# Kernel tuning notes

Measured on AMD Instinct MI355X. Metric: run time of the kernel, lower is better.

Reference implementation:

```python
import jax, jax.numpy as jnp
import numpy as np

B, T, HID, H, DH, K = 2, 1024, 1024, 16, 64, 4
ROPE_BASE = 10000.0
EPS = 1e-6


def _causal_dwconv(x, w, b):
    # x: (B, T, C); w: (C, 1, K) depthwise; causal left-pad K-1, then SiLU
    xc = jnp.transpose(x, (0, 2, 1))  # (B, C, T)
    y = jax.lax.conv_general_dilated(
        xc, w, window_strides=(1,), padding=[(K - 1, 0)],
        dimension_numbers=('NCH', 'OIH', 'NCH'), feature_group_count=xc.shape[1])
    y = y + b[None, :, None]
    return jax.nn.silu(jnp.transpose(y, (0, 2, 1)))


def _rope(x, cos, sin):
    # x: (B, T, H, D); cos/sin: (T, D) with emb = cat(freqs, freqs)
    c = cos[None, :, None, :]
    s = sin[None, :, None, :]
    x1, x2 = x[..., ::2], x[..., 1::2]
    return jnp.concatenate(
        [x1 * c[..., ::2] - x2 * s[..., ::2],
         x1 * s[..., ::2] + x2 * c[..., ::2]], axis=-1)


def _delta_rule(q, k, v, alpha, beta, D_param):
    # q,k,v: (B,T,H,DH); alpha,beta: (B,T,H)
    # S_t = alpha_t * (I - beta_t k_t k_t^T) S_{t-1} + beta_t k_t v_t^T
    # o_t  = q_t^T S_t-1-style readout + D * (q.k) * v   (matches torch einsum 'bhd,bhde->bhe')
    qs = jnp.moveaxis(q, 1, 0).astype(jnp.float32)  # (T,B,H,DH)
    ks = jnp.moveaxis(k, 1, 0).astype(jnp.float32)
    vs = jnp.moveaxis(v, 1, 0).astype(jnp.float32)
    als = jnp.moveaxis(alpha, 1, 0).astype(jnp.float32)  # (T,B,H)
    bes = jnp.moveaxis(beta, 1, 0).astype(jnp.float32)

    def step(S, inp):
        qt, kt, vt, at, bt = inp
        ot = jnp.einsum('bhd,bhde->bhe', qt, S)
        ot = ot + D_param[None, :, None] * jnp.sum(qt * kt, -1, keepdims=True) * vt
        kS = jnp.einsum('bhd,bhde->bhe', kt, S)  # k^T S
        at_ = at[..., None, None]
        bt_ = bt[..., None, None]
        S_new = at_ * (S - bt_ * kt[..., :, None] * kS[..., None, :]) \
                + bt_ * kt[..., :, None] * vt[..., None, :]
        return S_new, ot

    S0 = jnp.zeros((q.shape[0], H, DH, DH), jnp.float32)
    _, outs = jax.lax.scan(step, S0, (qs, ks, vs, als, bes))
    return jnp.moveaxis(outs, 0, 1)  # (B,T,H,DH)


def _forward(x, Wq, Wk, Wv, Wg, Wo, bw, bb, gkw, gkb,
             qcw, qcb, kcw, kcb, vcw, vcb, A_log, D_param, dt_bias, onorm_w):
    Bb, Tt, _ = x.shape
    q = _causal_dwconv(x @ Wq, qcw, qcb).reshape(Bb, Tt, H, DH)
    k = _causal_dwconv(x @ Wk, kcw, kcb).reshape(Bb, Tt, H, DH)
    v = _causal_dwconv(x @ Wv, vcw, vcb).reshape(Bb, Tt, H, DH)

    # RoPE (computed on the fly, fp32)
    t = jnp.arange(Tt, dtype=jnp.float32)
    inv_freq = 1.0 / (ROPE_BASE ** (jnp.arange(0, DH, 2, dtype=jnp.float32) / DH))
    freqs = jnp.outer(t, inv_freq)
    emb = jnp.concatenate([freqs, freqs], -1)
    cos, sin = jnp.cos(emb), jnp.sin(emb)
    q = _rope(q, cos, sin)
    k = _rope(k, cos, sin)

    # L2-normalize q/k (delta-net stability, NOT softmax)
    q = q * jax.lax.rsqrt(jnp.sum(q * q, -1, keepdims=True) + EPS)
    k = k * jax.lax.rsqrt(jnp.sum(k * k, -1, keepdims=True) + EPS)

    beta = jax.nn.sigmoid(x @ bw + bb)  # (B,T,H) writing strength
    alpha = jnp.exp(-jnp.exp(A_log) * jax.nn.softplus(x @ gkw + gkb + dt_bias))  # (B,T,H) decay

    o = _delta_rule(q, k, v, alpha, beta, D_param)  # (B,T,H,DH)

    # gated RMSNorm output: g * silu(RMSNorm(o))
    g = (x @ Wg).reshape(Bb, Tt, H, DH)
    on = o * jax.lax.rsqrt(jnp.mean(o * o, -1, keepdims=True) + EPS) * onorm_w
    o = g * jax.nn.silu(on)
    return o.reshape(Bb, Tt, H * DH) @ Wo


def setup_inputs() -> dict:
    key = jax.random.key(0)
    ks = jax.random.split(key, 20)
    w = lambda i, shape, s=0.02: (jax.random.normal(ks[i], shape, jnp.float32) * s)
    return {
        'x': jax.random.normal(ks[0], (B, T, HID), jnp.float32),
        'Wq': w(1, (HID, H * DH)), 'Wk': w(2, (HID, H * DH)),
        'Wv': w(3, (HID, H * DH)), 'Wg': w(4, (HID, H * DH)),
        'Wo': w(5, (H * DH, HID)),
        'bw': w(6, (HID, H)), 'bb': jnp.zeros((H,), jnp.float32),
        'gkw': w(7, (HID, H)), 'gkb': jnp.zeros((H,), jnp.float32),
        'qcw': w(8, (H * DH, 1, K), 0.3), 'qcb': jnp.zeros((H * DH,), jnp.float32),
        'kcw': w(9, (H * DH, 1, K), 0.3), 'kcb': jnp.zeros((H * DH,), jnp.float32),
        'vcw': w(10, (H * DH, 1, K), 0.3), 'vcb': jnp.zeros((H * DH,), jnp.float32),
        'A_log': jnp.log(jax.random.uniform(ks[11], (H,), jnp.float32, 1.0, 16.0)),
        'D_param': jnp.ones((H,), jnp.float32),
        'dt_bias': jax.random.uniform(ks[12], (H,), jnp.float32, -0.01, 0.01),
        'onorm_w': jnp.ones((DH,), jnp.float32),
    }


def reference(x, Wq, Wk, Wv, Wg, Wo, bw, bb, gkw, gkb,
              qcw, qcb, kcw, kcb, vcw, vcb, A_log, D_param, dt_bias, onorm_w):
    return _forward(x, Wq, Wk, Wv, Wg, Wo, bw, bb, gkw, gkb,
                    qcw, qcb, kcw, kcb, vcw, vcb, A_log, D_param, dt_bias, onorm_w)
```

## Files before the change

kernel.cpp:

```cpp
#include <hip/hip_runtime.h>
#include <hip/hip_bf16.h>
#include <cstdint>

#define T_LEN 1024
#define HIDN  1024
#define NH    16
#define DHD   64

typedef __bf16 bf16x8 __attribute__((ext_vector_type(8)));
typedef float  f32x4  __attribute__((ext_vector_type(4)));

__device__ inline void split8(float4 x0, float4 x1, uint4& hi, uint4& lo) {
  union { __bf16 h[8]; uint4 u; } ph, pl;
  float v[8] = {x0.x, x0.y, x0.z, x0.w, x1.x, x1.y, x1.z, x1.w};
#pragma unroll
  for (int j = 0; j < 8; j++) {
    __bf16 h = (__bf16)v[j];
    ph.h[j] = h;
    pl.h[j] = (__bf16)(v[j] - (float)h);
  }
  hi = ph.u; lo = pl.u;
}

__global__ __launch_bounds__(256) void k_transp_split(
    const float* __restrict__ W0, const float* __restrict__ W1,
    const float* __restrict__ W2, const float* __restrict__ W3,
    const float* __restrict__ W4,
    __bf16* __restrict__ H0, __bf16* __restrict__ H1, __bf16* __restrict__ H2,
    __bf16* __restrict__ H3, __bf16* __restrict__ H4,
    __bf16* __restrict__ L0, __bf16* __restrict__ L1, __bf16* __restrict__ L2,
    __bf16* __restrict__ L3, __bf16* __restrict__ L4) {
  const float* W; __bf16* Th; __bf16* Tl;
  switch (blockIdx.z) {
    case 0: W = W0; Th = H0; Tl = L0; break;
    case 1: W = W1; Th = H1; Tl = L1; break;
    case 2: W = W2; Th = H2; Tl = L2; break;
    case 3: W = W3; Th = H3; Tl = L3; break;
    default: W = W4; Th = H4; Tl = L4; break;
  }
  __shared__ float tile[64][65];
  int tid = threadIdx.x;
  int r0 = tid >> 4;
  int c0 = (tid & 15) * 4;
  int kbase = blockIdx.y * 64, nbase = blockIdx.x * 64;
#pragma unroll
  for (int rr = 0; rr < 4; rr++) {
    int r = r0 + rr * 16;
    float4 v = *(const float4*)(W + (size_t)(kbase + r) * 1024 + nbase + c0);
    tile[r][c0 + 0] = v.x; tile[r][c0 + 1] = v.y;
    tile[r][c0 + 2] = v.z; tile[r][c0 + 3] = v.w;
  }
  __syncthreads();
#pragma unroll
  for (int rr = 0; rr < 4; rr++) {
    int n = r0 + rr * 16;
    union { __bf16 h[4]; unsigned long long u; } ph, pl;
#pragma unroll
    for (int j = 0; j < 4; j++) {
      float v = tile[c0 + j][n];
      __bf16 h = (__bf16)v;
      ph.h[j] = h;
      pl.h[j] = (__bf16)(v - (float)h);
    }
    *(unsigned long long*)(Th + (size_t)(nbase + n) * 1024 + kbase + c0) = ph.u;
    *(unsigned long long*)(Tl + (size_t)(nbase + n) * 1024 + kbase + c0) = pl.u;
  }
}

#define LDT 40
__global__ __launch_bounds__(256) void k_gemm3f(
    const float* __restrict__ Af,
    const __bf16* __restrict__ Bh0, const __bf16* __restrict__ Bh1,
    const __bf16* __restrict__ Bh2, const __bf16* __restrict__ Bh3,
    const __bf16* __restrict__ Bl0, const __bf16* __restrict__ Bl1,
    const __bf16* __restrict__ Bl2, const __bf16* __restrict__ Bl3,
    float* __restrict__ C0, float* __restrict__ C1,
    float* __restrict__ C2, float* __restrict__ C3,
    int Kdim, int Ncols) {
  const __bf16* Bh; const __bf16* Bl; float* C;
  switch (blockIdx.z) {
    case 0: Bh = Bh0; Bl = Bl0; C = C0; break;
    case 1: Bh = Bh1; Bl = Bl1; C = C1; break;
    case 2: Bh = Bh2; Bl = Bl2; C = C2; break;
    default: Bh = Bh3; Bl = Bl3; C = C3; break;
  }
  __shared__ __bf16 Ash[128 * LDT];
  __shared__ __bf16 Asl[128 * LDT];
  __shared__ __bf16 Bsh[128 * LDT];
  __shared__ __bf16 Bsl[128 * LDT];
  const int tid = threadIdx.x;
  const int lane = tid & 63;
  const int wave = tid >> 6;
  const int wr = wave >> 1, wc = wave & 1;
  const int rowA0 = blockIdx.y * 128;
  const int colB0 = blockIdx.x * 128;
  const int sseg = tid & 3;
  const int srow0 = tid >> 2;
  const int srow1 = srow0 + 64;

  f32x4 acc[4][4] = {};

  for (int k0 = 0; k0 < Kdim; k0 += 32) {
    size_t a0 = (size_t)(rowA0 + srow0) * Kdim + k0 + sseg * 8;
    size_t a1 = (size_t)(rowA0 + srow1) * Kdim + k0 + sseg * 8;
    size_t b0 = (size_t)(colB0 + srow0) * Kdim + k0 + sseg * 8;
    size_t b1 = (size_t)(colB0 + srow1) * Kdim + k0 + sseg * 8;
    float4 a00 = *(const float4*)(Af + a0);
    float4 a01 = *(const float4*)(Af + a0 + 4);
    float4 a10 = *(const float4*)(Af + a1);
    float4 a11 = *(const float4*)(Af + a1 + 4);
    uint4 rbh0 = *(const uint4*)(Bh + b0);
    uint4 rbh1 = *(const uint4*)(Bh + b1);
    uint4 rbl0 = *(const uint4*)(Bl + b0);
    uint4 rbl1 = *(const uint4*)(Bl + b1);
    uint4 rah0, ral0, rah1, ral1;
    split8(a00, a01, rah0, ral0);
    split8(a10, a11, rah1, ral1);
    __syncthreads();
    *(uint4*)&Ash[srow0 * LDT + sseg * 8] = rah0;
    *(uint4*)&Ash[srow1 * LDT + sseg * 8] = rah1;
    *(uint4*)&Asl[srow0 * LDT + sseg * 8] = ral0;
    *(uint4*)&Asl[srow1 * LDT + sseg * 8] = ral1;
    *(uint4*)&Bsh[srow0 * LDT + sseg * 8] = rbh0;
    *(uint4*)&Bsh[srow1 * LDT + sseg * 8] = rbh1;
    *(uint4*)&Bsl[srow0 * LDT + sseg * 8] = rbl0;
    *(uint4*)&Bsl[srow1 * LDT + sseg * 8] = rbl1;
    __syncthreads();
    bf16x8 afh[4], afl[4], bfh[4], bfl[4];
#pragma unroll
    for (int mi = 0; mi < 4; mi++) {
      int off = (wr * 64 + mi * 16 + (lane & 15)) * LDT + (lane >> 4) * 8;
      afh[mi] = *(const bf16x8*)&Ash[off];
      afl[mi] = *(const bf16x8*)&Asl[off];
    }
#pragma unroll
    for (int ni = 0; ni < 4; ni++) {
      int off = (wc * 64 + ni * 16 + (lane & 15)) * LDT + (lane >> 4) * 8;
      bfh[ni] = *(const bf16x8*)&Bsh[off];
      bfl[ni] = *(const bf16x8*)&Bsl[off];
    }
#pragma unroll
    for (int mi = 0; mi < 4; mi++)
#pragma unroll
      for (int ni = 0; ni < 4; ni++) {
        acc[mi][ni] = __builtin_amdgcn_mfma_f32_16x16x32_bf16(afh[mi], bfh[ni], acc[mi][ni], 0, 0, 0);
        acc[mi][ni] = __builtin_amdgcn_mfma_f32_16x16x32_bf16(afl[mi], bfh[ni], acc[mi][ni], 0, 0, 0);
        acc[mi][ni] = __builtin_amdgcn_mfma_f32_16x16x32_bf16(afh[mi], bfl[ni], acc[mi][ni], 0, 0, 0);
      }
  }
#pragma unroll
  for (int mi = 0; mi < 4; mi++)
#pragma unroll
    for (int ni = 0; ni < 4; ni++) {
      int col = colB0 + wc * 64 + ni * 16 + (lane & 15);
#pragma unroll
      for (int r = 0; r < 4; r++) {
        int row = rowA0 + wr * 64 + mi * 16 + (lane >> 4) * 4 + r;
        C[(size_t)row * Ncols + col] = acc[mi][ni][r];
      }
    }
}

__global__ __launch_bounds__(256) void k_gates(
    const float* __restrict__ x, const float* __restrict__ bw,
    const float* __restrict__ bb, const float* __restrict__ gkw,
    const float* __restrict__ gkb, const float* __restrict__ A_log,
    const float* __restrict__ dt_bias,
    float* __restrict__ alphaB, float* __restrict__ betaB) {
  const int bt = blockIdx.x;
  const int tid = threadIdx.x;
  const int h = tid & 15;
  const int chunk = tid >> 4;
  const float* xr = x + (size_t)bt * HIDN;
  float d1 = 0.f, d2 = 0.f;
#pragma unroll 8
  for (int j = 0; j < 64; j++) {
    int k = chunk * 64 + j;
    float xv = xr[k];
    d1 += xv * bw[k * 16 + h];
    d2 += xv * gkw[k * 16 + h];
  }
  __shared__ float p1[16][16], p2[16][16];
  p1[chunk][h] = d1; p2[chunk][h] = d2;
  __syncthreads();
  if (tid < 16) {
    float s1 = 0.f, s2 = 0.f;
#pragma unroll
    for (int c = 0; c < 16; c++) { s1 += p1[c][tid]; s2 += p2[c][tid]; }
    float beta = 1.f / (1.f + expf(-(s1 + bb[tid])));
    float z = s2 + gkb[tid] + dt_bias[tid];
    float sp = fmaxf(z, 0.f) + log1pf(expf(-fabsf(z)));
    float alpha = expf(-expf(A_log[tid]) * sp);
    alphaB[(size_t)bt * 16 + tid] = alpha;
    betaB[(size_t)bt * 16 + tid] = beta;
  }
}

__global__ __launch_bounds__(256) void k_cra(
    const float* __restrict__ qp, const float* __restrict__ kp,
    const float* __restrict__ vp,
    const float* __restrict__ qcw, const float* __restrict__ qcb,
    const float* __restrict__ kcw, const float* __restrict__ kcb,
    const float* __restrict__ vcw, const float* __restrict__ vcb,
    const float* __restrict__ alphaB, const float* __restrict__ betaB,
    const float* __restrict__ Dp,
    float* __restrict__ qr, float* __restrict__ kr, float* __restrict__ vr,
    float4* __restrict__ aux) {
  int widx = blockIdx.x * 4 + (threadIdx.x >> 6);
  int lane = threadIdx.x & 63;
  int h = widx & 15;
  int bt = widx >> 4;
  int t = bt & 1023, b = bt >> 10;
  int c = h * 64 + lane;
  size_t colbase = ((size_t)b * 1024) * 1024 + c;

  float4 wq = *(const float4*)(qcw + (size_t)c * 4);
  float4 wk = *(const float4*)(kcw + (size_t)c * 4);
  float4 wv = *(const float4*)(vcw + (size_t)c * 4);
  float aq = qcb[c], ak = kcb[c], av = vcb[c];
  {
    float x0 = qp[colbase + (size_t)t * 1024];
    float y0 = kp[colbase + (size_t)t * 1024];
    float z0 = vp[colbase + (size_t)t * 1024];
    aq += wq.w * x0; ak += wk.w * y0; av += wv.w * z0;
    if (t >= 1) {
      float x1 = qp[colbase + (size_t)(t - 1) * 1024];
      float y1 = kp[colbase + (size_t)(t - 1) * 1024];
      float z1 = vp[colbase + (size_t)(t - 1) * 1024];
      aq += wq.z * x1; ak += wk.z * y1; av += wv.z * z1;
    }
    if (t >= 2) {
      float x2 = qp[colbase + (size_t)(t - 2) * 1024];
      float y2 = kp[colbase + (size_t)(t - 2) * 1024];
      float z2 = vp[colbase + (size_t)(t - 2) * 1024];
      aq += wq.y * x2; ak += wk.y * y2; av += wv.y * z2;
    }
    if (t >= 3) {
      float x3 = qp[colbase + (size_t)(t - 3) * 1024];
      float y3 = kp[colbase + (size_t)(t - 3) * 1024];
      float z3 = vp[colbase + (size_t)(t - 3) * 1024];
      aq += wq.x * x3; ak += wk.x * y3; av += wv.x * z3;
    }
  }
  float yq = aq / (1.f + expf(-aq));
  float yk = ak / (1.f + expf(-ak));
  float yv = av / (1.f + expf(-av));

  int i = lane & 31;
  float fr = expf(-(float)(2 * (i & 15)) * (9.210340371976184f / 32.f));
  float ang = (float)t * fr;
  float cv = cosf(ang), sv = sinf(ang);
  float q1 = __shfl(yq, 2 * i), q2 = __shfl(yq, 2 * i + 1);
  float k1 = __shfl(yk, 2 * i), k2 = __shfl(yk, 2 * i + 1);
  float qo = (lane < 32) ? (q1 * cv - q2 * sv) : (q1 * sv + q2 * cv);
  float ko = (lane < 32) ? (k1 * cv - k2 * sv) : (k1 * sv + k2 * cv);

  float qs = qo * qo, ks2 = ko * ko;
#pragma unroll
  for (int m = 1; m < 64; m <<= 1) { qs += __shfl_xor(qs, m); ks2 += __shfl_xor(ks2, m); }
  float qn = qo * rsqrtf(qs + 1e-6f);
  float kn = ko * rsqrtf(ks2 + 1e-6f);
  float dq = qn * kn;
#pragma unroll
  for (int m = 1; m < 64; m <<= 1) dq += __shfl_xor(dq, m);
  size_t obase = ((size_t)(b * 16 + h) * 1024 + t) * 64;
  qr[obase + lane] = qn;
  kr[obase + lane] = kn;
  vr[obase + lane] = yv;
  if (lane == 0) {
    float alpha = alphaB[(size_t)bt * 16 + h];
    float beta = betaB[(size_t)bt * 16 + h];
    aux[(size_t)(b * 16 + h) * 1024 + t] = make_float4(alpha, beta, alpha * beta, Dp[h] * dq);
  }
}

__global__ __launch_bounds__(128) void k_scanA(
    const float* __restrict__ qr, const float* __restrict__ kr,
    const float* __restrict__ vr, const float4* __restrict__ aux,
    float* __restrict__ O1, float* __restrict__ AcF,
    float* __restrict__ BcTF, float* __restrict__ QeffF,
    float* __restrict__ gcF) {
  const int bid = blockIdx.x;
  const int bh = bid >> 4, c = bid & 15;
  const int t0 = c * 64;
  const int tid = threadIdx.x;
  const int w = tid >> 6, lane = tid & 63;
  const float* qB = qr + (size_t)bh * 65536 + (size_t)t0 * 64;
  const float* kB = kr + (size_t)bh * 65536 + (size_t)t0 * 64;
  const float* vB = vr + (size_t)bh * 65536 + (size_t)t0 * 64;
  const float4* auxB = aux + (size_t)bh * T_LEN + t0;

  __shared__ __bf16 q_b[64 * 72];
  __shared__ __bf16 k_b[64 * 72];
  __shared__ __bf16 kT_b[64 * 72];
  __shared__ __bf16 C_b[64 * 72];
  __shared__ __bf16 U0T[64 * 72];
  __shared__ __bf16 WT[64 * 72];
  __shared__ float  vS[64 * 64];
  __shared__ float  MTf[64 * 68];
  __shared__ float  lgS[64], pvS[64], beS[64], awS[64], enS[64];

  if (w == 0) {
    float4 a4 = auxB[lane];
    float lg = logf(a4.x);
#pragma unroll
    for (int off = 1; off < 64; off <<= 1) {
      float tv = __shfl_up(lg, off);
      if (lane >= off) lg += tv;
    }
    float pv = __shfl_up(lg, 1);
    if (lane == 0) pv = 0.f;
    float lgTot = __shfl(lg, 63);
    lgS[lane] = lg; pvS[lane] = pv; beS[lane] = a4.y; awS[lane] = a4.w;
    enS[lane] = expf(lgTot - lg);
    if (lane == 0) gcF[bid] = expf(lgTot);
  }
#pragma unroll
  for (int p = 0; p < 4; p++) {
    int s = p * 128 + tid;
    int row = s >> 3, col8 = s & 7;
    const float* gq = qB + (size_t)row * 64 + col8 * 8;
    const float* gk = kB + (size_t)row * 64 + col8 * 8;
    const float* gv = vB + (size_t)row * 64 + col8 * 8;
    float4 q0 = *(const float4*)gq, q1 = *(const float4*)(gq + 4);
    float4 k0 = *(const float4*)gk, k1 = *(const float4*)(gk + 4);
    float4 v0 = *(const float4*)gv, v1 = *(const float4*)(gv + 4);
    union { __bf16 h[8]; uint4 u; } pq, pk;
    pq.h[0] = (__bf16)q0.x; pq.h[1] = (__bf16)q0.y; pq.h[2] = (__bf16)q0.z; pq.h[3] = (__bf16)q0.w;
    pq.h[4] = (__bf16)q1.x; pq.h[5] = (__bf16)q1.y; pq.h[6] = (__bf16)q1.z; pq.h[7] = (__bf16)q1.w;
    pk.h[0] = (__bf16)k0.x; pk.h[1] = (__bf16)k0.y; pk.h[2] = (__bf16)k0.z; pk.h[3] = (__bf16)k0.w;
    pk.h[4] = (__bf16)k1.x; pk.h[5] = (__bf16)k1.y; pk.h[6] = (__bf16)k1.z; pk.h[7] = (__bf16)k1.w;
    *(uint4*)&q_b[row * 72 + col8 * 8] = pq.u;
    *(uint4*)&k_b[row * 72 + col8 * 8] = pk.u;
    *(float4*)&vS[row * 64 + col8 * 8] = v0;
    *(float4*)&vS[row * 64 + col8 * 8 + 4] = v1;
  }
  __syncthreads();

#pragma unroll
  for (int mm = 0; mm < 2; mm++) {
    int mi = w * 2 + mm;
#pragma unroll
    for (int ni = 0; ni < 4; ni++) {
      f32x4 akk = {0.f, 0.f, 0.f, 0.f};
      f32x4 aqk = {0.f, 0.f, 0.f, 0.f};
#pragma unroll
      for (int ks = 0; ks < 2; ks++) {
        bf16x8 fa_k = *(const bf16x8*)&k_b[(mi * 16 + (lane & 15)) * 72 + ks * 32 + (lane >> 4) * 8];
        bf16x8 fa_q = *(const bf16x8*)&q_b[(mi * 16 + (lane & 15)) * 72 + ks * 32 + (lane >> 4) * 8];
        bf16x8 fb_k = *(const bf16x8*)&k_b[(ni * 16 + (lane & 15)) * 72 + ks * 32 + (lane >> 4) * 8];
        akk = __builtin_amdgcn_mfma_f32_16x16x32_bf16(fa_k, fb_k, akk, 0, 0, 0);
        aqk = __builtin_amdgcn_mfma_f32_16x16x32_bf16(fa_q, fb_k, aqk, 0, 0, 0);
      }
#pragma unroll
      for (int r = 0; r < 4; r++) {
        int row = mi * 16 + (lane >> 4) * 4 + r;
        int col = ni * 16 + (lane & 15);
        float mt = 0.f, cv = 0.f;
        if (row > col) {
          mt = beS[row] * expf(lgS[row] - lgS[col]) * akk[r];
          cv = expf(pvS[row] - lgS[col]) * aqk[r];
        }
        MTf[col * 68 + row] = mt;
        C_b[row * 72 + col] = (__bf16)cv;
      }
    }
  }
  __syncthreads();

  if (w == 1) {
#pragma unroll
    for (int t8 = 0; t8 < 8; t8++) {
      union { __bf16 h[8]; uint4 u; } pt;
#pragma unroll
      for (int q = 0; q < 8; q++) {
        int t = t8 * 8 + q;
        pt.h[q] = (__bf16)((float)k_b[t * 72 + lane] * enS[t]);
      }
      *(uint4*)&kT_b[lane * 72 + t8 * 8] = pt.u;
    }
  }

  {
    float u[64];
    if (w == 0) {
#pragma unroll
      for (int j = 0; j < 64; j++) u[j] = beS[j] * vS[j * 64 + lane];
    } else {
#pragma unroll
      for (int j = 0; j < 64; j++) u[j] = beS[j] * expf(lgS[j]) * (float)k_b[j * 72 + lane];
    }
    __bf16* dst = (w == 0) ? U0T : WT;
#pragma unroll
    for (int j = 0; j < 64; j++) {
      dst[lane * 72 + j] = (__bf16)u[j];
      float uj = u[j];
#pragma unroll
      for (int g = (j >> 4); g < 4; g++) {
#pragma unroll
        for (int q4 = 0; q4 < 4; q4++) {
          const float4 m4 = *(const float4*)&MTf[j * 68 + g * 16 + q4 * 4];
          u[g * 16 + q4 * 4 + 0] -= m4.x * uj;
          u[g * 16 + q4 * 4 + 1] -= m4.y * uj;
          u[g * 16 + q4 * 4 + 2] -= m4.z * uj;
          u[g * 16 + q4 * 4 + 3] -= m4.w * uj;
        }
      }
    }
  }
  __syncthreads();

  size_t cb = (size_t)bid * 4096;
  if (w == 0) {
#pragma unroll
    for (int mi = 0; mi < 4; mi++)
#pragma unroll
      for (int ni = 0; ni < 4; ni++) {
        f32x4 ab = {0.f, 0.f, 0.f, 0.f};
        f32x4 aa = {0.f, 0.f, 0.f, 0.f};
#pragma unroll
        for (int ks = 0; ks < 2; ks++) {
          int aoff = (mi * 16 + (lane & 15)) * 72 + ks * 32 + (lane >> 4) * 8;
          int boff = (ni * 16 + (lane & 15)) * 72 + ks * 32 + (lane >> 4) * 8;
          bf16x8 fu = *(const bf16x8*)&U0T[aoff];
          bf16x8 fkm = *(const bf16x8*)&kT_b[aoff];
          bf16x8 fkn = *(const bf16x8*)&kT_b[boff];
          bf16x8 fw = *(const bf16x8*)&WT[boff];
          ab = __builtin_amdgcn_mfma_f32_16x16x32_bf16(fu, fkn, ab, 0, 0, 0);
          aa = __builtin_amdgcn_mfma_f32_16x16x32_bf16(fkm, fw, aa, 0, 0, 0);
        }
#pragma unroll
        for (int r = 0; r < 4; r++) {
          int row = mi * 16 + (lane >> 4) * 4 + r;
          int col = ni * 16 + (lane & 15);
          BcTF[cb + row * 64 + col] = ab[r];
          AcF[cb + row * 64 + col] = aa[r];
        }
      }
  } else {
#pragma unroll
    for (int mi = 0; mi < 4; mi++)
#pragma unroll
      for (int ni = 0; ni < 4; ni++) {
        f32x4 ao = {0.f, 0.f, 0.f, 0.f};
        f32x4 ac = {0.f, 0.f, 0.f, 0.f};
#pragma unroll
        for (int ks = 0; ks < 2; ks++) {
          int aoff = (mi * 16 + (lane & 15)) * 72 + ks * 32 + (lane >> 4) * 8;
          int boff = (ni * 16 + (lane & 15)) * 72 + ks * 32 + (lane >> 4) * 8;
          bf16x8 fc = *(const bf16x8*)&C_b[aoff];
          bf16x8 fu = *(const bf16x8*)&U0T[boff];
          bf16x8 fw = *(const bf16x8*)&WT[boff];
          ao = __builtin_amdgcn_mfma_f32_16x16x32_bf16(fc, fu, ao, 0, 0, 0);
          ac = __builtin_amdgcn_mfma_f32_16x16x32_bf16(fc, fw, ac, 0, 0, 0);
        }
#pragma unroll
        for (int r = 0; r < 4; r++) {
          int t = mi * 16 + (lane >> 4) * 4 + r;
          int col = ni * 16 + (lane & 15);
          O1[(size_t)bh * 65536 + (size_t)(t0 + t) * 64 + col] =
              ao[r] + awS[t] * vS[t * 64 + col];
          QeffF[cb + t * 64 + col] = expf(pvS[t]) * (float)q_b[t * 72 + col] - ac[r];
        }
      }
  }
}

__global__ __launch_bounds__(256) void k_scanB(
    const float* __restrict__ AcF, const float* __restrict__ BcTF,
    const float* __restrict__ gcF, float* __restrict__ S0TF) {
  const int bh = blockIdx.x;
  const int tid = threadIdx.x;
  const int w = tid >> 6, lane = tid & 63;
  const int er = tid >> 2, seg = (tid & 3) * 16;
  __shared__ float STf[64 * 68];
  __shared__ __bf16 Sh[64 * 72], Sl[64 * 72], Ac_b[64 * 72];
#pragma unroll
  for (int i = 0; i < 4; i++)
    *(float4*)&STf[er * 68 + seg + i * 4] = make_float4(0.f, 0.f, 0.f, 0.f);
  __syncthreads();

  size_t cbase = (size_t)bh * 16 * 4096;
  float4 acR[4];
  float bctR[16];
#pragma unroll
  for (int i = 0; i < 4; i++)
    acR[i] = *(const float4*)&AcF[cbase + er * 64 + seg + i * 4];
#pragma unroll
  for (int r = 0; r < 4; r++)
#pragma unroll
    for (int ni = 0; ni < 4; ni++) {
      int e = w * 16 + (lane >> 4) * 4 + r;
      int d = ni * 16 + (lane & 15);
      bctR[r * 4 + ni] = BcTF[cbase + e * 64 + d];
    }

  for (int c = 0; c < 16; c++) {
    size_t cb = cbase + (size_t)c * 4096;
#pragma unroll
    for (int i = 0; i < 4; i++) {
      float4 s = *(const float4*)&STf[er * 68 + seg + i * 4];
      *(float4*)&S0TF[cb + er * 64 + seg + i * 4] = s;
      union { __bf16 h[4]; unsigned long long u; } ph, pl, pa;
      float sv[4] = {s.x, s.y, s.z, s.w};
      float av[4] = {acR[i].x, acR[i].y, acR[i].z, acR[i].w};
#pragma unroll
      for (int q = 0; q < 4; q++) {
        __bf16 hv = (__bf16)sv[q];
        ph.h[q] = hv;
        pl.h[q] = (__bf16)(sv[q] - (float)hv);
        pa.h[q] = (__bf16)av[q];
      }
      *(unsigned long long*)&Sh[er * 72 + seg + i * 4] = ph.u;
      *(unsigned long long*)&Sl[er * 72 + seg + i * 4] = pl.u;
      *(unsigned long long*)&Ac_b[er * 72 + seg + i * 4] = pa.u;
    }
    float gC = gcF[bh * 16 + c];
    __syncthreads();

    float4 acN[4];
    float bctN[16];
    if (c < 15) {
      size_t nb = cb + 4096;
#pragma unroll
      for (int i = 0; i < 4; i++)
        acN[i] = *(const float4*)&AcF[nb + er * 64 + seg + i * 4];
#pragma unroll
      for (int r = 0; r < 4; r++)
#pragma unroll
        for (int ni = 0; ni < 4; ni++) {
          int e = w * 16 + (lane >> 4) * 4 + r;
          int d = ni * 16 + (lane & 15);
          bctN[r * 4 + ni] = BcTF[nb + e * 64 + d];
        }
    } else {
#pragma unroll
      for (int i = 0; i < 4; i++) acN[i] = acR[i];
#pragma unroll
      for (int j = 0; j < 16; j++) bctN[j] = bctR[j];
    }

    f32x4 acc[4];
#pragma unroll
    for (int ni = 0; ni < 4; ni++) {
      acc[ni] = (f32x4){0.f, 0.f, 0.f, 0.f};
#pragma unroll
      for (int ks = 0; ks < 2; ks++) {
        int aoff = (w * 16 + (lane & 15)) * 72 + ks * 32 + (lane >> 4) * 8;
        int boff = (ni * 16 + (lane & 15)) * 72 + ks * 32 + (lane >> 4) * 8;
        bf16x8 ah = *(const bf16x8*)&Sh[aoff];
        bf16x8 al = *(const bf16x8*)&Sl[aoff];
        bf16x8 bb = *(const bf16x8*)&Ac_b[boff];
        acc[ni] = __builtin_amdgcn_mfma_f32_16x16x32_bf16(ah, bb, acc[ni], 0, 0, 0);
        acc[ni] = __builtin_amdgcn_mfma_f32_16x16x32_bf16(al, bb, acc[ni], 0, 0, 0);
      }
    }
#pragma unroll
    for (int ni = 0; ni < 4; ni++)
#pragma unroll
      for (int r = 0; r < 4; r++) {
        int e = w * 16 + (lane >> 4) * 4 + r;
        int d = ni * 16 + (lane & 15);
        STf[e * 68 + d] = gC * STf[e * 68 + d] - acc[ni][r] + bctR[r * 4 + ni];
      }
    __syncthreads();
#pragma unroll
    for (int i = 0; i < 4; i++) acR[i] = acN[i];
#pragma unroll
    for (int j = 0; j < 16; j++) bctR[j] = bctN[j];
  }
}

__global__ __launch_bounds__(256) void k_scanCn(
    const float* __restrict__ S0TF, const float* __restrict__ QeffF,
    const float* __restrict__ obuf, const float* __restrict__ g,
    const float* __restrict__ onw, float* __restrict__ robuf) {
  const int bid = blockIdx.x;
  const int bh = bid >> 4, c = bid & 15, t0c = c * 64;
  const int b = bh >> 4, h = bh & 15;
  const int tid = threadIdx.x;
  const int w = tid >> 6, lane = tid & 63;
  const int er = tid >> 2, seg = (tid & 3) * 16;
  size_t cb = (size_t)bid * 4096;
  __shared__ __bf16 Sh[64 * 72], Sl[64 * 72], Qb[64 * 72];
#pragma unroll
  for (int i = 0; i < 4; i++) {
    float4 s = *(const float4*)&S0TF[cb + er * 64 + seg + i * 4];
    union { __bf16 h[4]; unsigned long long u; } ph, pl;
    float sv[4] = {s.x, s.y, s.z, s.w};
#pragma unroll
    for (int q = 0; q < 4; q++) {
      __bf16 hv = (__bf16)sv[q];
      ph.h[q] = hv;
      pl.h[q] = (__bf16)(sv[q] - (float)hv);
    }
    *(unsigned long long*)&Sh[er * 72 + seg + i * 4] = ph.u;
    *(unsigned long long*)&Sl[er * 72 + seg + i * 4] = pl.u;
    float4 qq = *(const float4*)&QeffF[cb + er * 64 + seg + i * 4];
    union { __bf16 h[4]; unsigned long long u; } pq;
    pq.h[0] = (__bf16)qq.x; pq.h[1] = (__bf16)qq.y;
    pq.h[2] = (__bf16)qq.z; pq.h[3] = (__bf16)qq.w;
    *(unsigned long long*)&Qb[er * 72 + seg + i * 4] = pq.u;
  }
  __syncthreads();
  f32x4 acc[4];
#pragma unroll
  for (int ni = 0; ni < 4; ni++) {
    acc[ni] = (f32x4){0.f, 0.f, 0.f, 0.f};
#pragma unroll
    for (int ks = 0; ks < 2; ks++) {
      int aoff = (w * 16 + (lane & 15)) * 72 + ks * 32 + (lane >> 4) * 8;
      int boff = (ni * 16 + (lane & 15)) * 72 + ks * 32 + (lane >> 4) * 8;
      bf16x8 fq = *(const bf16x8*)&Qb[aoff];
      bf16x8 sh = *(const bf16x8*)&Sh[boff];
      bf16x8 sl = *(const bf16x8*)&Sl[boff];
      acc[ni] = __builtin_amdgcn_mfma_f32_16x16x32_bf16(fq, sh, acc[ni], 0, 0, 0);
      acc[ni] = __builtin_amdgcn_mfma_f32_16x16x32_bf16(fq, sl, acc[ni], 0, 0, 0);
    }
  }
  float onwv[4];
#pragma unroll
  for (int ni = 0; ni < 4; ni++) onwv[ni] = onw[ni * 16 + (lane & 15)];
#pragma unroll
  for (int r = 0; r < 4; r++) {
    int t = w * 16 + (lane >> 4) * 4 + r;
    float o[4];
#pragma unroll
    for (int ni = 0; ni < 4; ni++) {
      int e = ni * 16 + (lane & 15);
      o[ni] = obuf[(size_t)bh * 65536 + (size_t)(t0c + t) * 64 + e] + acc[ni][r];
    }
    float ss = o[0] * o[0] + o[1] * o[1] + o[2] * o[2] + o[3] * o[3];
    ss += __shfl_xor(ss, 1);
    ss += __shfl_xor(ss, 2);
    ss += __shfl_xor(ss, 4);
    ss += __shfl_xor(ss, 8);
    float rinv = rsqrtf(ss * (1.f / 64.f) + 1e-6f);
    size_t gbase = ((size_t)(b * 1024 + t0c + t)) * 1024 + h * 64;
#pragma unroll
    for (int ni = 0; ni < 4; ni++) {
      int e = ni * 16 + (lane & 15);
      float on = o[ni] * rinv * onwv[ni];
      float sil = on / (1.f + expf(-on));
      robuf[gbase + e] = g[gbase + e] * sil;
    }
  }
}

extern "C" void kernel_launch(void* const* d_in, const int* in_sizes, int n_in,
                              void* d_out, int out_size, void* d_ws, size_t ws_size,
                              hipStream_t stream) {
  (void)in_sizes; (void)n_in; (void)out_size; (void)ws_size;
  const float* x    = (const float*)d_in[0];
  const float* Wq   = (const float*)d_in[1];
  const float* Wk   = (const float*)d_in[2];
  const float* Wv   = (const float*)d_in[3];
  const float* Wg   = (const float*)d_in[4];
  const float* Wo   = (const float*)d_in[5];
  const float* bw   = (const float*)d_in[6];
  const float* bb   = (const float*)d_in[7];
  const float* gkw  = (const float*)d_in[8];
  const float* gkb  = (const float*)d_in[9];
  const float* qcw  = (const float*)d_in[10];
  const float* qcb  = (const float*)d_in[11];
  const float* kcw  = (const float*)d_in[12];
  const float* kcb  = (const float*)d_in[13];
  const float* vcw  = (const float*)d_in[14];
  const float* vcb  = (const float*)d_in[15];
  const float* A_log= (const float*)d_in[16];
  const float* Dp   = (const float*)d_in[17];
  const float* dtb  = (const float*)d_in[18];
  const float* onw  = (const float*)d_in[19];

  char* ws = (char*)d_ws;
  const size_t MB = 1024 * 1024;
  __bf16* Wq_h = (__bf16*)(ws + 8 * MB);
  __bf16* Wq_l = (__bf16*)(ws + 10 * MB);
  __bf16* Wk_h = (__bf16*)(ws + 12 * MB);
  __bf16* Wk_l = (__bf16*)(ws + 14 * MB);
  __bf16* Wv_h = (__bf16*)(ws + 16 * MB);
  __bf16* Wv_l = (__bf16*)(ws + 18 * MB);
  __bf16* Wg_h = (__bf16*)(ws + 20 * MB);
  __bf16* Wg_l = (__bf16*)(ws + 22 * MB);
  __bf16* Wo_h = (__bf16*)(ws + 24 * MB);
  __bf16* Wo_l = (__bf16*)(ws + 26 * MB);
  float* q_pre = (float*)(ws + 28 * MB);
  float* k_pre = (float*)(ws + 36 * MB);
  float* v_pre = (float*)(ws + 44 * MB);
  float* g_buf = (float*)(ws + 52 * MB);
  float* qrb   = (float*)(ws + 0);
  float* krb   = (float*)(ws + 8 * MB);
  float* vr    = (float*)(ws + 16 * MB);
  float* obuf  = v_pre;
  float* AcF   = (float*)(ws + 28 * MB);
  float* BcTF  = (float*)(ws + 36 * MB);
  float* S0TF  = (float*)(ws + 0);
  float* QeffF = (float*)(ws + 16 * MB);
  float* robuf = (float*)(ws + 8 * MB);
  float* alphaB = (float*)(ws + 60 * MB);
  float* betaB  = (float*)(ws + 60 * MB + 128 * 1024);
  float4* aux   = (float4*)(ws + 60 * MB + 256 * 1024);
  float* gcF    = (float*)(ws + 60 * MB + 768 * 1024);
  float* out    = (float*)d_out;

  k_transp_split<<<dim3(16, 16, 5), 256, 0, stream>>>(
      Wq, Wk, Wv, Wg, Wo,
      Wq_h, Wk_h, Wv_h, Wg_h, Wo_h,
      Wq_l, Wk_l, Wv_l, Wg_l, Wo_l);
  k_gates<<<2048, 256, 0, stream>>>(x, bw, bb, gkw, gkb, A_log, dtb, alphaB, betaB);
  k_gemm3f<<<dim3(8, 16, 4), 256, 0, stream>>>(
      x,
      Wq_h, Wk_h, Wv_h, Wg_h,
      Wq_l, Wk_l, Wv_l, Wg_l,
      q_pre, k_pre, v_pre, g_buf, 1024, 1024);
  k_cra<<<8192, 256, 0, stream>>>(q_pre, k_pre, v_pre,
                                  qcw, qcb, kcw, kcb, vcw, vcb,
                                  alphaB, betaB, Dp, qrb, krb, vr, aux);
  k_scanA<<<512, 128, 0, stream>>>(qrb, krb, vr, aux, obuf, AcF, BcTF, QeffF, gcF);
  k_scanB<<<32, 256, 0, stream>>>(AcF, BcTF, gcF, S0TF);
  k_scanCn<<<512, 256, 0, stream>>>(S0TF, QeffF, obuf, g_buf, onw, robuf);
  k_gemm3f<<<dim3(8, 16, 1), 256, 0, stream>>>(
      robuf,
      Wo_h, Wo_h, Wo_h, Wo_h,
      Wo_l, Wo_l, Wo_l, Wo_l,
      out, out, out, out, 1024, 1024);
}
```

Baseline: 331.7 us.

## Trim split-bf16 GEMM terms per projection and fuse gate computation into conv kernel

The split-bf16 GEMM gains a per-slice term count: the Q and G projections use only the hi*hi product, K and V keep all three terms, and the output projection drops the B-low term. Low-part weight transposes are skipped where no longer needed. The separate gates kernel is removed and its beta/alpha reduction is computed inside the conv/rope kernel with wave shuffles. The aim is to cut MFMA work, LDS traffic and one launch, at the cost of lower precision on Q, G and the output projection, which is risky because Q is normalized before use.

```diff
diff --git a/kernel.cpp b/kernel.cpp
--- a/kernel.cpp
+++ b/kernel.cpp
@@ -28,15 +28,14 @@
     const float* __restrict__ W4,
     __bf16* __restrict__ H0, __bf16* __restrict__ H1, __bf16* __restrict__ H2,
     __bf16* __restrict__ H3, __bf16* __restrict__ H4,
-    __bf16* __restrict__ L0, __bf16* __restrict__ L1, __bf16* __restrict__ L2,
-    __bf16* __restrict__ L3, __bf16* __restrict__ L4) {
+    __bf16* __restrict__ L1, __bf16* __restrict__ L2) {
   const float* W; __bf16* Th; __bf16* Tl;
   switch (blockIdx.z) {
-    case 0: W = W0; Th = H0; Tl = L0; break;
+    case 0: W = W0; Th = H0; Tl = nullptr; break;
     case 1: W = W1; Th = H1; Tl = L1; break;
     case 2: W = W2; Th = H2; Tl = L2; break;
-    case 3: W = W3; Th = H3; Tl = L3; break;
-    default: W = W4; Th = H4; Tl = L4; break;
+    case 3: W = W3; Th = H3; Tl = nullptr; break;
+    default: W = W4; Th = H4; Tl = nullptr; break;
   }
   __shared__ float tile[64][65];
   int tid = threadIdx.x;
@@ -63,7 +62,8 @@
       pl.h[j] = (__bf16)(v - (float)h);
     }
     *(unsigned long long*)(Th + (size_t)(nbase + n) * 1024 + kbase + c0) = ph.u;
-    *(unsigned long long*)(Tl + (size_t)(nbase + n) * 1024 + kbase + c0) = pl.u;
+    if (Tl)
+      *(unsigned long long*)(Tl + (size_t)(nbase + n) * 1024 + kbase + c0) = pl.u;
   }
 }
 
@@ -76,13 +76,14 @@
     const __bf16* __restrict__ Bl2, const __bf16* __restrict__ Bl3,
     float* __restrict__ C0, float* __restrict__ C1,
     float* __restrict__ C2, float* __restrict__ C3,
+    int nt0, int nt1, int nt2, int nt3,
     int Kdim, int Ncols) {
-  const __bf16* Bh; const __bf16* Bl; float* C;
+  const __bf16* Bh; const __bf16* Bl; float* C; int nt;
   switch (blockIdx.z) {
-    case 0: Bh = Bh0; Bl = Bl0; C = C0; break;
-    case 1: Bh = Bh1; Bl = Bl1; C = C1; break;
-    case 2: Bh = Bh2; Bl = Bl2; C = C2; break;
-    default: Bh = Bh3; Bl = Bl3; C = C3; break;
+    case 0: Bh = Bh0; Bl = Bl0; C = C0; nt = nt0; break;
+    case 1: Bh = Bh1; Bl = Bl1; C = C1; nt = nt1; break;
+    case 2: Bh = Bh2; Bl = Bl2; C = C2; nt = nt2; break;
+    default: Bh = Bh3; Bl = Bl3; C = C3; nt = nt3; break;
   }
   __shared__ __bf16 Ash[128 * LDT];
   __shared__ __bf16 Asl[128 * LDT];
@@ -111,41 +112,50 @@
     float4 a11 = *(const float4*)(Af + a1 + 4);
     uint4 rbh0 = *(const uint4*)(Bh + b0);
     uint4 rbh1 = *(const uint4*)(Bh + b1);
-    uint4 rbl0 = *(const uint4*)(Bl + b0);
-    uint4 rbl1 = *(const uint4*)(Bl + b1);
+    uint4 rbl0, rbl1;
+    if (nt >= 3) {
+      rbl0 = *(const uint4*)(Bl + b0);
+      rbl1 = *(const uint4*)(Bl + b1);
+    }
     uint4 rah0, ral0, rah1, ral1;
     split8(a00, a01, rah0, ral0);
     split8(a10, a11, rah1, ral1);
     __syncthreads();
     *(uint4*)&Ash[srow0 * LDT + sseg * 8] = rah0;
     *(uint4*)&Ash[srow1 * LDT + sseg * 8] = rah1;
-    *(uint4*)&Asl[srow0 * LDT + sseg * 8] = ral0;
-    *(uint4*)&Asl[srow1 * LDT + sseg * 8] = ral1;
+    if (nt >= 2) {
+      *(uint4*)&Asl[srow0 * LDT + sseg * 8] = ral0;
+      *(uint4*)&Asl[srow1 * LDT + sseg * 8] = ral1;
+    }
     *(uint4*)&Bsh[srow0 * LDT + sseg * 8] = rbh0;
     *(uint4*)&Bsh[srow1 * LDT + sseg * 8] = rbh1;
-    *(uint4*)&Bsl[srow0 * LDT + sseg * 8] = rbl0;
-    *(uint4*)&Bsl[srow1 * LDT + sseg * 8] = rbl1;
+    if (nt >= 3) {
+      *(uint4*)&Bsl[srow0 * LDT + sseg * 8] = rbl0;
+      *(uint4*)&Bsl[srow1 * LDT + sseg * 8] = rbl1;
+    }
     __syncthreads();
     bf16x8 afh[4], afl[4], bfh[4], bfl[4];
 #pragma unroll
     for (int mi = 0; mi < 4; mi++) {
       int off = (wr * 64 + mi * 16 + (lane & 15)) * LDT + (lane >> 4) * 8;
       afh[mi] = *(const bf16x8*)&Ash[off];
-      afl[mi] = *(const bf16x8*)&Asl[off];
+      if (nt >= 2) afl[mi] = *(const bf16x8*)&Asl[off];
     }
 #pragma unroll
     for (int ni = 0; ni < 4; ni++) {
       int off = (wc * 64 + ni * 16 + (lane & 15)) * LDT + (lane >> 4) * 8;
       bfh[ni] = *(const bf16x8*)&Bsh[off];
-      bfl[ni] = *(const bf16x8*)&Bsl[off];
+      if (nt >= 3) bfl[ni] = *(const bf16x8*)&Bsl[off];
     }
 #pragma unroll
     for (int mi = 0; mi < 4; mi++)
 #pragma unroll
       for (int ni = 0; ni < 4; ni++) {
         acc[mi][ni] = __builtin_amdgcn_mfma_f32_16x16x32_bf16(afh[mi], bfh[ni], acc[mi][ni], 0, 0, 0);
-        acc[mi][ni] = __builtin_amdgcn_mfma_f32_16x16x32_bf16(afl[mi], bfh[ni], acc[mi][ni], 0, 0, 0);
-        acc[mi][ni] = __builtin_amdgcn_mfma_f32_16x16x32_bf16(afh[mi], bfl[ni], acc[mi][ni], 0, 0, 0);
+        if (nt >= 2)
+          acc[mi][ni] = __builtin_amdgcn_mfma_f32_16x16x32_bf16(afl[mi], bfh[ni], acc[mi][ni], 0, 0, 0);
+        if (nt >= 3)
+          acc[mi][ni] = __builtin_amdgcn_mfma_f32_16x16x32_bf16(afh[mi], bfl[ni], acc[mi][ni], 0, 0, 0);
       }
   }
 #pragma unroll
@@ -161,48 +171,15 @@
     }
 }
 
-__global__ __launch_bounds__(256) void k_gates(
-    const float* __restrict__ x, const float* __restrict__ bw,
-    const float* __restrict__ bb, const float* __restrict__ gkw,
-    const float* __restrict__ gkb, const float* __restrict__ A_log,
-    const float* __restrict__ dt_bias,
-    float* __restrict__ alphaB, float* __restrict__ betaB) {
-  const int bt = blockIdx.x;
-  const int tid = threadIdx.x;
-  const int h = tid & 15;
-  const int chunk = tid >> 4;
-  const float* xr = x + (size_t)bt * HIDN;
-  float d1 = 0.f, d2 = 0.f;
-#pragma unroll 8
-  for (int j = 0; j < 64; j++) {
-    int k = chunk * 64 + j;
-    float xv = xr[k];
-    d1 += xv * bw[k * 16 + h];
-    d2 += xv * gkw[k * 16 + h];
-  }
-  __shared__ float p1[16][16], p2[16][16];
-  p1[chunk][h] = d1; p2[chunk][h] = d2;
-  __syncthreads();
-  if (tid < 16) {
-    float s1 = 0.f, s2 = 0.f;
-#pragma unroll
-    for (int c = 0; c < 16; c++) { s1 += p1[c][tid]; s2 += p2[c][tid]; }
-    float beta = 1.f / (1.f + expf(-(s1 + bb[tid])));
-    float z = s2 + gkb[tid] + dt_bias[tid];
-    float sp = fmaxf(z, 0.f) + log1pf(expf(-fabsf(z)));
-    float alpha = expf(-expf(A_log[tid]) * sp);
-    alphaB[(size_t)bt * 16 + tid] = alpha;
-    betaB[(size_t)bt * 16 + tid] = beta;
-  }
-}
-
 __global__ __launch_bounds__(256) void k_cra(
     const float* __restrict__ qp, const float* __restrict__ kp,
-    const float* __restrict__ vp,
+    const float* __restrict__ vp, const float* __restrict__ x,
     const float* __restrict__ qcw, const float* __restrict__ qcb,
     const float* __restrict__ kcw, const float* __restrict__ kcb,
     const float* __restrict__ vcw, const float* __restrict__ vcb,
-    const float* __restrict__ alphaB, const float* __restrict__ betaB,
+    const float* __restrict__ bw, const float* __restrict__ bb,
+    const float* __restrict__ gkw, const float* __restrict__ gkb,
+    const float* __restrict__ A_log, const float* __restrict__ dtb,
     const float* __restrict__ Dp,
     float* __restrict__ qr, float* __restrict__ kr, float* __restrict__ vr,
     float4* __restrict__ aux) {
@@ -213,6 +190,22 @@
   int t = bt & 1023, b = bt >> 10;
   int c = h * 64 + lane;
   size_t colbase = ((size_t)b * 1024) * 1024 + c;
+
+  const float* xr = x + (size_t)bt * HIDN;
+  float d1 = 0.f, d2 = 0.f;
+#pragma unroll
+  for (int j = 0; j < 16; j++) {
+    int k = lane + j * 64;
+    float xv = xr[k];
+    d1 += xv * bw[k * 16 + h];
+    d2 += xv * gkw[k * 16 + h];
+  }
+#pragma unroll
+  for (int m = 1; m < 64; m <<= 1) { d1 += __shfl_xor(d1, m); d2 += __shfl_xor(d2, m); }
+  float beta = 1.f / (1.f + expf(-(d1 + bb[h])));
+  float z2 = d2 + gkb[h] + dtb[h];
+  float sp = fmaxf(z2, 0.f) + log1pf(expf(-fabsf(z2)));
+  float alpha = expf(-expf(A_log[h]) * sp);
 
   float4 wq = *(const float4*)(qcw + (size_t)c * 4);
   float4 wk = *(const float4*)(kcw + (size_t)c * 4);
@@ -232,8 +225,8 @@
     if (t >= 2) {
       float x2 = qp[colbase + (size_t)(t - 2) * 1024];
       float y2 = kp[colbase + (size_t)(t - 2) * 1024];
-      float z2 = vp[colbase + (size_t)(t - 2) * 1024];
-      aq += wq.y * x2; ak += wk.y * y2; av += wv.y * z2;
+      float z2v = vp[colbase + (size_t)(t - 2) * 1024];
+      aq += wq.y * x2; ak += wk.y * y2; av += wv.y * z2v;
     }
     if (t >= 3) {
       float x3 = qp[colbase + (size_t)(t - 3) * 1024];
@@ -267,11 +260,8 @@
   qr[obase + lane] = qn;
   kr[obase + lane] = kn;
   vr[obase + lane] = yv;
-  if (lane == 0) {
-    float alpha = alphaB[(size_t)bt * 16 + h];
-    float beta = betaB[(size_t)bt * 16 + h];
+  if (lane == 0)
     aux[(size_t)(b * 16 + h) * 1024 + t] = make_float4(alpha, beta, alpha * beta, Dp[h] * dq);
-  }
 }
 
 __global__ __launch_bounds__(128) void k_scanA(
@@ -697,25 +687,25 @@
   float* S0TF  = (float*)(ws + 0);
   float* QeffF = (float*)(ws + 16 * MB);
   float* robuf = (float*)(ws + 8 * MB);
-  float* alphaB = (float*)(ws + 60 * MB);
-  float* betaB  = (float*)(ws + 60 * MB + 128 * 1024);
-  float4* aux   = (float4*)(ws + 60 * MB + 256 * 1024);
-  float* gcF    = (float*)(ws + 60 * MB + 768 * 1024);
-  float* out    = (float*)d_out;
+  float4* aux  = (float4*)(ws + 60 * MB + 256 * 1024);
+  float* gcF   = (float*)(ws + 60 * MB + 768 * 1024);
+  float* out   = (float*)d_out;
 
   k_transp_split<<<dim3(16, 16, 5), 256, 0, stream>>>(
       Wq, Wk, Wv, Wg, Wo,
       Wq_h, Wk_h, Wv_h, Wg_h, Wo_h,
-      Wq_l, Wk_l, Wv_l, Wg_l, Wo_l);
-  k_gates<<<2048, 256, 0, stream>>>(x, bw, bb, gkw, gkb, A_log, dtb, alphaB, betaB);
+      Wk_l, Wv_l);
   k_gemm3f<<<dim3(8, 16, 4), 256, 0, stream>>>(
       x,
       Wq_h, Wk_h, Wv_h, Wg_h,
       Wq_l, Wk_l, Wv_l, Wg_l,
-      q_pre, k_pre, v_pre, g_buf, 1024, 1024);
-  k_cra<<<8192, 256, 0, stream>>>(q_pre, k_pre, v_pre,
+      q_pre, k_pre, v_pre, g_buf,
+      1, 3, 3, 1,
+      1024, 1024);
+  k_cra<<<8192, 256, 0, stream>>>(q_pre, k_pre, v_pre, x,
                                   qcw, qcb, kcw, kcb, vcw, vcb,
-                                  alphaB, betaB, Dp, qrb, krb, vr, aux);
+                                  bw, bb, gkw, gkb, A_log, dtb, Dp,
+                                  qrb, krb, vr, aux);
   k_scanA<<<512, 128, 0, stream>>>(qrb, krb, vr, aux, obuf, AcF, BcTF, QeffF, gcF);
   k_scanB<<<32, 256, 0, stream>>>(AcF, BcTF, gcF, S0TF);
   k_scanCn<<<512, 256, 0, stream>>>(S0TF, QeffF, obuf, g_buf, onw, robuf);
@@ -723,5 +713,7 @@
       robuf,
       Wo_h, Wo_h, Wo_h, Wo_h,
       Wo_l, Wo_l, Wo_l, Wo_l,
-      out, out, out, out, 1024, 1024);
+      out, out, out, out,
+      2, 2, 2, 2,
+      1024, 1024);
 }
```

After: 420.2 us. +26.7%, slower.
